# Kernel tuning notes

Hardware: AMD Instinct MI355X
Metric: run time of the kernel (lower is better)

Reference implementation:

```python
import jax, jax.numpy as jnp
import numpy as np


def _lstm_scan(xs, W_ih, W_hh, b, h0, c0):
    """Run an LSTMCell over time. xs: [T, B, D]; returns (hs [T,B,H], h_T, c_T).
    PyTorch LSTMCell gate order: i, f, g, o; b = b_ih + b_hh fused."""
    H = h0.shape[-1]

    def step(carry, x_t):
        h, c = carry
        gates = x_t @ W_ih.T + h @ W_hh.T + b  # [B, 4H]
        i, f, g, o = jnp.split(gates, 4, axis=-1)
        i = jax.nn.sigmoid(i)
        f = jax.nn.sigmoid(f)
        g = jnp.tanh(g)
        o = jax.nn.sigmoid(o)
        c_new = f * c + i * g
        h_new = o * jnp.tanh(c_new)
        return (h_new, c_new), h_new

    (h_T, c_T), hs = jax.lax.scan(step, (h0, c0), xs)
    return hs, h_T, c_T


def setup_inputs() -> dict:
    key = jax.random.key(0)
    ks = jax.random.split(key, 7)
    B, T, F, H = 64, 512, 256, 1024
    s = lambda fan_in: np.sqrt(2.0) * np.sqrt(6.0 / (4 * H + fan_in))  # xavier_uniform gain=sqrt(2)
    return {
        "x": jax.random.normal(ks[0], (B, T, F), dtype=jnp.float32),
        "W_ih_e": jax.random.uniform(ks[1], (4 * H, F), jnp.float32, -s(F), s(F)),
        "W_hh_e": jax.random.uniform(ks[2], (4 * H, H), jnp.float32, -s(H), s(H)),
        "b_e": jnp.zeros((4 * H,), jnp.float32),
        "W_ih_d": jax.random.uniform(ks[3], (4 * H, H), jnp.float32, -s(H), s(H)),
        "W_hh_d": jax.random.uniform(ks[4], (4 * H, H), jnp.float32, -s(H), s(H)),
        "b_d": jnp.zeros((4 * H,), jnp.float32),
        "W_out": jax.random.uniform(ks[5], (F, H), jnp.float32, -s(F), s(F)),
        "b_out": jnp.zeros((F,), jnp.float32),
    }


def reference(x, W_ih_e, W_hh_e, b_e, W_ih_d, W_hh_d, b_d, W_out, b_out):
    B, T, F = x.shape
    H = W_hh_e.shape[1]
    xs = jnp.swapaxes(x, 0, 1)  # [T, B, F] time-major
    h0 = jnp.zeros((B, H), x.dtype)
    c0 = jnp.zeros((B, H), x.dtype)
    # Encoder: LSTMCell(F, H), collect per-step hidden states
    enc_hs, h_T, c_T = _lstm_scan(xs, W_ih_e, W_hh_e, b_e, h0, c0)  # [T, B, H]
    # Decoder: LSTMCell(H, H) over encoder hidden states, seeded with final (h, c)
    dec_hs, _, _ = _lstm_scan(enc_hs, W_ih_d, W_hh_d, b_d, h_T, c_T)  # [T, B, H]
    # Output projection H -> F
    out = jnp.einsum('tbh,fh->tbf', dec_hs, W_out) + b_out
    return jnp.swapaxes(out, 0, 1)  # [B, T, F]
```

## Files before the change

kernel.cpp:

```cpp
#include <hip/hip_runtime.h>
#include <math.h>

#define TT 512
#define BB 64
#define FF 256
#define HH 1024
#define NBLK 256
#define NCHE 5
#define NCHD 8

typedef __attribute__((ext_vector_type(8))) short short8;
typedef __attribute__((ext_vector_type(4))) float f32x4;

__device__ __forceinline__ unsigned short f2bf(float f) {
    unsigned u = __float_as_uint(f);
    u += 0x7FFFu + ((u >> 16) & 1u);
    return (unsigned short)(u >> 16);
}
__device__ __forceinline__ float bf2f(unsigned short u) {
    return __uint_as_float((unsigned)u << 16);
}

__global__ __launch_bounds__(256) void k_cast_x(const float* __restrict__ x,
                                                unsigned short* __restrict__ xB) {
    int t = blockIdx.x;
    #pragma unroll
    for (int i = 0; i < 16; ++i) {
        int id = threadIdx.x + i * 256;
        int b  = id >> 6;
        int f4 = (id & 63) << 2;
        float4 v = *(const float4*)(x + ((size_t)b * TT + t) * FF + f4);
        ushort4 o;
        o.x = f2bf(v.x); o.y = f2bf(v.y); o.z = f2bf(v.z); o.w = f2bf(v.w);
        *(ushort4*)(xB + ((size_t)t * BB + b) * FF + f4) = o;
    }
}

__global__ __launch_bounds__(256) void k_wcast(const float* __restrict__ in,
                                               unsigned short* __restrict__ out,
                                               int n4) {
    int stride = gridDim.x * 256;
    for (int i = blockIdx.x * 256 + threadIdx.x; i < n4; i += stride) {
        float4 v = ((const float4*)in)[i];
        ushort4 o;
        o.x = f2bf(v.x); o.y = f2bf(v.y); o.z = f2bf(v.z); o.w = f2bf(v.w);
        ((ushort4*)out)[i] = o;
    }
}

__device__ __forceinline__ void publish(unsigned* __restrict__ flags,
                                        int widx, unsigned val) {
    asm volatile("s_waitcnt vmcnt(0)" ::: "memory");
    if ((threadIdx.x & 63) == 0)
        __hip_atomic_store(flags + widx, val, __ATOMIC_RELAXED,
                           __HIP_MEMORY_SCOPE_AGENT);
}

__device__ __forceinline__ void waitall16(const unsigned* __restrict__ mir,
                                          int mpage, int lane, unsigned tgt) {
    const unsigned long long* line =
        (const unsigned long long*)(mir + mpage * 64);
    for (;;) {
        unsigned long long v = __hip_atomic_load(line + (lane & 7),
                                                 __ATOMIC_RELAXED,
                                                 __HIP_MEMORY_SCOPE_AGENT);
        bool ok = ((unsigned)v >= tgt) && ((unsigned)(v >> 32) >= tgt);
        if (__all(ok)) break;
        __builtin_amdgcn_s_sleep(1);
    }
    asm volatile("" ::: "memory");
}

__device__ __forceinline__ void aggregator(unsigned* __restrict__ flags,
                                           unsigned* __restrict__ mir,
                                           int g, int lane) {
    for (unsigned e = 1; e <= 2u * TT - 1; ++e) {
        for (;;) {
            unsigned v = __hip_atomic_load(flags + g * 64 + lane,
                                           __ATOMIC_RELAXED,
                                           __HIP_MEMORY_SCOPE_AGENT);
            if (__all(v >= e)) break;
            __builtin_amdgcn_s_sleep(1);
        }
        if (lane < 8)
            __hip_atomic_store(mir + lane * 64 + g, e, __ATOMIC_RELAXED,
                               __HIP_MEMORY_SCOPE_AGENT);
        asm volatile("s_waitcnt vmcnt(0)" ::: "memory");
    }
}

template <int NCH, int C1>
__device__ __forceinline__ void lstm_step(
    const short8* __restrict__ sW,
    const unsigned short* __restrict__ A1, int K1,
    const unsigned short* __restrict__ A2, int K2,
    const f32x4 bias, float& creg,
    unsigned short* __restrict__ hOut,
    unsigned* __restrict__ flags, unsigned* __restrict__ mir,
    int tgt, int widx, unsigned pub, int mpage,
    int lane, int q, int n, int j0, int u, int b)
{
    short8 av[3][8];
    auto aload = [&](short8* dst, int c) {
        const unsigned short* ap = (c < C1)
            ? A1 + (size_t)b * K1 + (size_t)c * 256
            : A2 + (size_t)b * K2 + (size_t)(c - C1) * 256;
        ap += q * 8;
        #pragma unroll
        for (int f = 0; f < 8; ++f) dst[f] = *(const short8*)(ap + f * 32);
    };

    f32x4 accA = {0.f, 0.f, 0.f, 0.f};
    f32x4 accB = {0.f, 0.f, 0.f, 0.f};

    aload(av[0], 0);
    if (C1 > 1) aload(av[1], 1);
    #pragma unroll
    for (int c = 0; c < C1; ++c) {
        if (c + 2 < C1) aload(av[(c + 2) % 3], c + 2);
        const short8* cur = av[c % 3];
        #pragma unroll
        for (int f = 0; f < 8; ++f) {
            short8 wv = sW[(c * 8 + f) * 64 + lane];
            if (f & 1) accB = __builtin_amdgcn_mfma_f32_16x16x32_bf16(wv, cur[f], accB, 0, 0, 0);
            else       accA = __builtin_amdgcn_mfma_f32_16x16x32_bf16(wv, cur[f], accA, 0, 0, 0);
        }
    }

    if (tgt > 0) waitall16(mir, mpage, lane, (unsigned)tgt);

    if (NCH > C1) {
        aload(av[C1 % 3], C1);
        if (NCH > C1 + 1) aload(av[(C1 + 1) % 3], C1 + 1);
        #pragma unroll
        for (int c = C1; c < NCH; ++c) {
            if (c + 2 < NCH) aload(av[(c + 2) % 3], c + 2);
            const short8* cur = av[c % 3];
            #pragma unroll
            for (int f = 0; f < 8; ++f) {
                short8 wv = sW[(c * 8 + f) * 64 + lane];
                if (f & 1) accB = __builtin_amdgcn_mfma_f32_16x16x32_bf16(wv, cur[f], accB, 0, 0, 0);
                else       accA = __builtin_amdgcn_mfma_f32_16x16x32_bf16(wv, cur[f], accA, 0, 0, 0);
            }
        }
    }
    f32x4 acc = accA + accB;

    float pi = acc[0] + bias[0];
    float pf = acc[1] + bias[1];
    float pg = acc[2] + bias[2];
    float po = acc[3] + bias[3];
    float iv = 1.f / (1.f + __expf(-pi));
    float fv = 1.f / (1.f + __expf(-pf));
    float gv = tanhf(pg);
    float ov = 1.f / (1.f + __expf(-po));
    float cn = fv * creg + iv * gv;
    creg = cn;
    float hn = ov * tanhf(cn);

    unsigned hv = (unsigned)f2bf(hn);
    unsigned v0 = (unsigned)__shfl((int)hv, n);
    unsigned v1 = (unsigned)__shfl((int)hv, n + 16);
    unsigned v2 = (unsigned)__shfl((int)hv, n + 32);
    unsigned v3 = (unsigned)__shfl((int)hv, n + 48);
    if (q == 0) {
        unsigned long long pk = (unsigned long long)(v0 | (v1 << 16)) |
                                ((unsigned long long)(v2 | (v3 << 16)) << 32);
        __hip_atomic_store((unsigned long long*)(hOut + (size_t)b * HH + j0), pk,
                           __ATOMIC_RELAXED, __HIP_MEMORY_SCOPE_AGENT);
    }
    if (pub) publish(flags, widx, pub);
}

__global__ __launch_bounds__(320, 1) void k_lstm_persist(
    const unsigned short* __restrict__ xB,
    const unsigned short* __restrict__ WihE,
    const unsigned short* __restrict__ WhhE,
    const float* __restrict__ bE,
    const unsigned short* __restrict__ WihD,
    const unsigned short* __restrict__ WhhD,
    const float* __restrict__ bD,
    unsigned short* __restrict__ encB,
    unsigned short* __restrict__ decR,
    unsigned* __restrict__ flags)
{
    __shared__ short8 sWe[NCHE * 8 * 64];
    __shared__ short8 sWd[NCHD * 8 * 64];

    const int tid  = threadIdx.x;
    const int lane = tid & 63;
    const int w    = tid >> 6;
    unsigned* mir  = flags + 1024;

    if (w == 4) {
        __syncthreads();
        if ((blockIdx.x & 15) == 0)
            aggregator(flags, mir, blockIdx.x >> 4, lane);
        return;
    }

    const int q    = lane >> 4;
    const int n    = lane & 15;
    const int j0   = blockIdx.x * 4;
    const int rrow = (n & 3) * HH + j0 + (n >> 2);
    const size_t SB = (size_t)BB * HH;
    const int widx  = blockIdx.x * 4 + w;
    const int mpage = blockIdx.x & 7;

    #pragma unroll
    for (int i = 0; i < 2 * NCHE; ++i) {
        int g = i * 4 + w;
        int c = g >> 3, f = g & 7;
        const unsigned short* Wp; int Ks; int cl;
        if (c < 1) { Wp = WihE; Ks = FF; cl = c; }
        else       { Wp = WhhE; Ks = HH; cl = c - 1; }
        sWe[g * 64 + lane] =
            *(const short8*)(Wp + (size_t)rrow * Ks + (size_t)cl * 256 + f * 32 + q * 8);
    }
    #pragma unroll
    for (int i = 0; i < 2 * NCHD; ++i) {
        int g = i * 4 + w;
        int c = g >> 3, f = g & 7;
        const unsigned short* Wp; int cl;
        if (c < 4) { Wp = WihD; cl = c; }
        else       { Wp = WhhD; cl = c - 4; }
        sWd[g * 64 + lane] =
            *(const short8*)(Wp + (size_t)rrow * HH + (size_t)cl * 256 + f * 32 + q * 8);
    }
    __syncthreads();

    const int u = j0 + q;
    const int b = w * 16 + n;
    const f32x4 biasE = {bE[u], bE[HH + u], bE[2 * HH + u], bE[3 * HH + u]};
    const f32x4 biasD = {bD[u], bD[HH + u], bD[2 * HH + u], bD[3 * HH + u]};

    float creg = 0.f;

    lstm_step<1, 1>(sWe, xB, FF, xB, FF, biasE, creg,
                    encB, flags, mir, 0, widx, 1u, mpage,
                    lane, q, n, j0, u, b);
    for (int t = 1; t < TT; ++t) {
        lstm_step<NCHE, 1>(sWe, xB + (size_t)t * BB * FF, FF,
                           encB + (size_t)(t - 1) * SB, HH,
                           biasE, creg, encB + (size_t)t * SB,
                           flags, mir, t, widx, (unsigned)(t + 1), mpage,
                           lane, q, n, j0, u, b);
    }

    for (int t = 0; t < TT; ++t) {
        const unsigned short* A2 = (t == 0) ? encB + (size_t)(TT - 1) * SB
                                            : decR + (size_t)(t - 1) * SB;
        unsigned pub = (t == TT - 1) ? 0u : (unsigned)(TT + t + 1);
        lstm_step<NCHD, 4>(sWd, encB + (size_t)t * SB, HH, A2, HH,
                           biasD, creg, decR + (size_t)t * SB,
                           flags, mir, TT + t, widx, pub, mpage,
                           lane, q, n, j0, u, b);
    }
}

__global__ __launch_bounds__(256) void k_out_proj_r(
    const unsigned short* __restrict__ decR,
    const float* __restrict__ Wout,
    const float* __restrict__ bout,
    float* __restrict__ out)
{
    int t  = blockIdx.x;
    int fg = blockIdx.y;
    const int lane = threadIdx.x & 63;
    const int wv   = __builtin_amdgcn_readfirstlane(threadIdx.x >> 6);
    const int f0   = fg * 64 + wv * 16;
    const unsigned short* a = decR + ((size_t)t * BB + lane) * HH;

    float acc[16];
    #pragma unroll
    for (int i = 0; i < 16; ++i) acc[i] = bout[f0 + i];

    for (int k8 = 0; k8 < HH / 8; ++k8) {
        short8 hv8 = *(const short8*)(a + k8 * 8);
        #pragma unroll
        for (int uu = 0; uu < 8; ++uu) {
            float hv = bf2f((unsigned short)hv8[uu]);
            #pragma unroll
            for (int i = 0; i < 16; ++i)
                acc[i] = fmaf(Wout[(size_t)(f0 + i) * HH + k8 * 8 + uu], hv, acc[i]);
        }
    }

    float* op = out + ((size_t)lane * TT + t) * FF + f0;
    #pragma unroll
    for (int i = 0; i < 16; i += 4) {
        float4 v = make_float4(acc[i], acc[i + 1], acc[i + 2], acc[i + 3]);
        *(float4*)(op + i) = v;
    }
}

template <int NCH>
__global__ __launch_bounds__(256) void k_step_lds(
    const unsigned short* __restrict__ A1, const unsigned short* __restrict__ W1, int K1,
    const unsigned short* __restrict__ A2, const unsigned short* __restrict__ W2, int K2,
    int C1,
    const float* __restrict__ bias,
    float* __restrict__ Cbuf,
    unsigned short* __restrict__ hOut,
    float* __restrict__ chunkOut)
{
    __shared__ short8 sW[NCH * 8 * 64];

    const int tid  = threadIdx.x;
    const int lane = tid & 63;
    const int w    = tid >> 6;
    const int q    = lane >> 4;
    const int n    = lane & 15;
    const int j0   = blockIdx.x * 4;
    const int rrow = (n & 3) * HH + j0 + (n >> 2);

    short8 av[3][8];

    auto aload = [&](short8* dst, int c) {
        const unsigned short* ap = (c < C1)
            ? A1 + (size_t)(w * 16 + n) * K1 + (size_t)c * 256
            : A2 + (size_t)(w * 16 + n) * K2 + (size_t)(c - C1) * 256;
        ap += q * 8;
        #pragma unroll
        for (int f = 0; f < 8; ++f) dst[f] = *(const short8*)(ap + f * 32);
    };

    aload(av[0], 0);
    if (NCH > 1) aload(av[1], 1);

    #pragma unroll
    for (int i = 0; i < 2 * NCH; ++i) {
        int g = i * 4 + w;
        int c = g >> 3, f = g & 7;
        const unsigned short* Wp; int Ks; int cl;
        if (c < C1) { Wp = W1; Ks = K1; cl = c; }
        else        { Wp = W2; Ks = K2; cl = c - C1; }
        sW[g * 64 + lane] =
            *(const short8*)(Wp + (size_t)rrow * Ks + (size_t)cl * 256 + f * 32 + q * 8);
    }
    __syncthreads();

    f32x4 accA = {0.f, 0.f, 0.f, 0.f};
    f32x4 accB = {0.f, 0.f, 0.f, 0.f};
    #pragma unroll
    for (int c = 0; c < NCH; ++c) {
        if (c + 2 < NCH) aload(av[(c + 2) % 3], c + 2);
        const short8* cur = av[c % 3];
        #pragma unroll
        for (int f = 0; f < 8; ++f) {
            short8 wv = sW[(c * 8 + f) * 64 + lane];
            if (f & 1) accB = __builtin_amdgcn_mfma_f32_16x16x32_bf16(wv, cur[f], accB, 0, 0, 0);
            else       accA = __builtin_amdgcn_mfma_f32_16x16x32_bf16(wv, cur[f], accA, 0, 0, 0);
        }
    }
    f32x4 acc = accA + accB;

    const int u = j0 + q;
    const int b = w * 16 + n;
    float pi = acc[0] + bias[u];
    float pf = acc[1] + bias[HH + u];
    float pg = acc[2] + bias[2 * HH + u];
    float po = acc[3] + bias[3 * HH + u];
    float iv = 1.f / (1.f + __expf(-pi));
    float fv = 1.f / (1.f + __expf(-pf));
    float gv = tanhf(pg);
    float ov = 1.f / (1.f + __expf(-po));
    size_t cix = (size_t)u * BB + b;
    float c  = Cbuf[cix];
    float cn = fv * c + iv * gv;
    Cbuf[cix] = cn;
    float hn = ov * tanhf(cn);
    hOut[(size_t)b * HH + u] = f2bf(hn);
    if (chunkOut) chunkOut[cix] = hn;
}

__device__ __forceinline__ void seg_f32(const unsigned short* __restrict__ ap0,
                                        const float* __restrict__ wp0,
                                        int nch, f32x4& acc) {
    const unsigned short* ap = ap0;
    const float* wp = wp0;
    #pragma unroll 2
    for (int c = 0; c < nch; ++c) {
        float4 wa = *(const float4*)wp;
        float4 wb = *(const float4*)(wp + 4);
        short8 av = *(const short8*)ap;
        short8 wv;
        wv[0] = (short)f2bf(wa.x); wv[1] = (short)f2bf(wa.y);
        wv[2] = (short)f2bf(wa.z); wv[3] = (short)f2bf(wa.w);
        wv[4] = (short)f2bf(wb.x); wv[5] = (short)f2bf(wb.y);
        wv[6] = (short)f2bf(wb.z); wv[7] = (short)f2bf(wb.w);
        acc = __builtin_amdgcn_mfma_f32_16x16x32_bf16(wv, av, acc, 0, 0, 0);
        ap += 32; wp += 32;
    }
}

__global__ __launch_bounds__(256) void k_step_f32w(
    const unsigned short* __restrict__ A1, const float* __restrict__ W1, int K1,
    const unsigned short* __restrict__ A2, const float* __restrict__ W2, int K2,
    const float* __restrict__ bias,
    float* __restrict__ Cbuf, unsigned short* __restrict__ hOut,
    float* __restrict__ chunkOut)
{
    const int tid  = threadIdx.x;
    const int lane = tid & 63;
    const int w    = tid >> 6;
    const int q    = lane >> 4;
    const int n    = lane & 15;
    const int j0   = blockIdx.x * 4;
    const int rrow = (n & 3) * HH + j0 + (n >> 2);

    f32x4 acc = {0.f, 0.f, 0.f, 0.f};
    seg_f32(A1 + (size_t)(w * 16 + n) * K1 + q * 8,
            W1 + (size_t)rrow * K1 + q * 8, K1 >> 5, acc);
    if (K2)
        seg_f32(A2 + (size_t)(w * 16 + n) * HH + q * 8,
                W2 + (size_t)rrow * HH + q * 8, HH >> 5, acc);

    const int u = j0 + q;
    const int b = w * 16 + n;
    float pi = acc[0] + bias[u];
    float pf = acc[1] + bias[HH + u];
    float pg = acc[2] + bias[2 * HH + u];
    float po = acc[3] + bias[3 * HH + u];
    float iv = 1.f / (1.f + __expf(-pi));
    float fv = 1.f / (1.f + __expf(-pf));
    float gv = tanhf(pg);
    float ov = 1.f / (1.f + __expf(-po));
    size_t cix = (size_t)u * BB + b;
    float c  = Cbuf[cix];
    float cn = fv * c + iv * gv;
    Cbuf[cix] = cn;
    float hn = ov * tanhf(cn);
    hOut[(size_t)b * HH + u] = f2bf(hn);
    if (chunkOut) chunkOut[cix] = hn;
}

__global__ __launch_bounds__(256) void k_out_proj(
    const float* __restrict__ chunk,
    const float* __restrict__ Wout,
    const float* __restrict__ bout,
    float* __restrict__ out,
    int t0)
{
    int tl = blockIdx.x;
    int t  = t0 + tl;
    int fg = blockIdx.y;
    const int lane = threadIdx.x & 63;
    const int wv   = __builtin_amdgcn_readfirstlane(threadIdx.x >> 6);
    const int f0   = fg * 64 + wv * 16;
    const float* a = chunk + (size_t)tl * HH * BB;

    float acc[16];
    #pragma unroll
    for (int i = 0; i < 16; ++i) acc[i] = bout[f0 + i];

    for (int k = 0; k < HH; k += 4) {
        #pragma unroll
        for (int u = 0; u < 4; ++u) {
            float hv = a[(size_t)(k + u) * BB + lane];
            #pragma unroll
            for (int i = 0; i < 16; ++i)
                acc[i] = fmaf(Wout[(size_t)(f0 + i) * HH + k + u], hv, acc[i]);
        }
    }

    float* op = out + ((size_t)lane * TT + t) * FF + f0;
    #pragma unroll
    for (int i = 0; i < 16; i += 4) {
        float4 v = make_float4(acc[i], acc[i + 1], acc[i + 2], acc[i + 3]);
        *(float4*)(op + i) = v;
    }
}

extern "C" void kernel_launch(void* const* d_in, const int* in_sizes, int n_in,
                              void* d_out, int out_size, void* d_ws, size_t ws_size,
                              hipStream_t stream) {
    const float* x     = (const float*)d_in[0];
    const float* Wih_e = (const float*)d_in[1];
    const float* Whh_e = (const float*)d_in[2];
    const float* b_e   = (const float*)d_in[3];
    const float* Wih_d = (const float*)d_in[4];
    const float* Whh_d = (const float*)d_in[5];
    const float* b_d   = (const float*)d_in[6];
    const float* Wout  = (const float*)d_in[7];
    const float* bout  = (const float*)d_in[8];
    float* out = (float*)d_out;

    const size_t SB = (size_t)BB * HH;

    unsigned short* xB = (unsigned short*)d_out;

    {
        char* p = (char*)d_ws;
        unsigned* flags = (unsigned*)p; p += 8192;
        unsigned short* encB  = (unsigned short*)p; p += (size_t)TT * SB * 2;
        unsigned short* decR  = (unsigned short*)p; p += (size_t)TT * SB * 2;
        unsigned short* WihEb = (unsigned short*)p; p += (size_t)4 * HH * FF * 2;
        unsigned short* WhhEb = (unsigned short*)p; p += (size_t)4 * HH * HH * 2;
        unsigned short* WihDb = (unsigned short*)p; p += (size_t)4 * HH * HH * 2;
        unsigned short* WhhDb = (unsigned short*)p; p += (size_t)4 * HH * HH * 2;
        size_t need = (size_t)(p - (char*)d_ws);

        if (ws_size >= need) {
            hipMemsetAsync(flags, 0, 8192, stream);
            k_cast_x<<<TT, 256, 0, stream>>>(x, xB);
            k_wcast<<<1024, 256, 0, stream>>>(Wih_e, WihEb, 4 * HH * FF / 4);
            k_wcast<<<1024, 256, 0, stream>>>(Whh_e, WhhEb, 4 * HH * HH / 4);
            k_wcast<<<1024, 256, 0, stream>>>(Wih_d, WihDb, 4 * HH * HH / 4);
            k_wcast<<<1024, 256, 0, stream>>>(Whh_d, WhhDb, 4 * HH * HH / 4);

            void* args[] = {
                (void*)&xB, (void*)&WihEb, (void*)&WhhEb, (void*)&b_e,
                (void*)&WihDb, (void*)&WhhDb, (void*)&b_d,
                (void*)&encB, (void*)&decR, (void*)&flags};
            hipLaunchCooperativeKernel((const void*)k_lstm_persist,
                                       dim3(NBLK), dim3(320), args, 0, stream);

            k_out_proj_r<<<dim3(TT, 4), 256, 0, stream>>>(decR, Wout, bout, out);
            return;
        }
    }

    char* p = (char*)d_ws;
    unsigned short* encB  = (unsigned short*)p; p += (size_t)TT * SB * 2;
    unsigned short* dech0 = (unsigned short*)p; p += SB * 2;
    unsigned short* dech1 = (unsigned short*)p; p += SB * 2;
    float* cbuf = (float*)p; p += SB * 4;
    size_t used  = (size_t)(p - (char*)d_ws);
    size_t avail = ws_size > used ? ws_size - used : 0;

    const size_t WE_B = ((size_t)4 * HH * FF + (size_t)4 * HH * HH) * 2;
    const size_t WD_B = ((size_t)4 * HH * HH) * 2 * 2;
    const size_t CH8  = (size_t)8 * SB * 4;

    bool wbAll = (avail >= WE_B + WD_B + CH8);
    bool wbEnc = wbAll || (avail >= WE_B + CH8);

    unsigned short *WihEb = 0, *WhhEb = 0, *WihDb = 0, *WhhDb = 0;
    if (wbEnc) {
        WihEb = (unsigned short*)p; p += (size_t)4 * HH * FF * 2;
        WhhEb = (unsigned short*)p; p += (size_t)4 * HH * HH * 2;
        avail -= WE_B;
    }
    if (wbAll) {
        WihDb = (unsigned short*)p; p += (size_t)4 * HH * HH * 2;
        WhhDb = (unsigned short*)p; p += (size_t)4 * HH * HH * 2;
        avail -= WD_B;
    }
    int C = 8;
    if      (avail >= (size_t)64 * SB * 4) C = 64;
    else if (avail >= (size_t)32 * SB * 4) C = 32;
    else if (avail >= (size_t)16 * SB * 4) C = 16;
    float* chunk = (float*)p;

    hipMemsetAsync(cbuf, 0, SB * 4, stream);
    k_cast_x<<<TT, 256, 0, stream>>>(x, xB);
    if (wbEnc) {
        k_wcast<<<1024, 256, 0, stream>>>(Wih_e, WihEb, 4 * HH * FF / 4);
        k_wcast<<<1024, 256, 0, stream>>>(Whh_e, WhhEb, 4 * HH * HH / 4);
    }
    if (wbAll) {
        k_wcast<<<1024, 256, 0, stream>>>(Wih_d, WihDb, 4 * HH * HH / 4);
        k_wcast<<<1024, 256, 0, stream>>>(Whh_d, WhhDb, 4 * HH * HH / 4);
    }

    for (int t = 0; t < TT; ++t) {
        const unsigned short* A1 = xB + (size_t)t * BB * FF;
        const unsigned short* A2 = t ? encB + (size_t)(t - 1) * SB : (unsigned short*)0;
        unsigned short* hOut = encB + (size_t)t * SB;
        if (wbEnc) {
            if (t == 0)
                k_step_lds<1><<<256, 256, 0, stream>>>(A1, WihEb, FF, A2, WhhEb, HH,
                                                       1, b_e, cbuf, hOut, (float*)0);
            else
                k_step_lds<5><<<256, 256, 0, stream>>>(A1, WihEb, FF, A2, WhhEb, HH,
                                                       1, b_e, cbuf, hOut, (float*)0);
        } else {
            k_step_f32w<<<256, 256, 0, stream>>>(A1, Wih_e, FF, A2, Whh_e,
                                                 t ? HH : 0, b_e, cbuf, hOut, (float*)0);
        }
    }

    for (int t = 0; t < TT; ++t) {
        const unsigned short* A1 = encB + (size_t)t * SB;
        const unsigned short* A2 = (t == 0) ? encB + (size_t)(TT - 1) * SB
                                            : ((t & 1) ? dech1 : dech0);
        unsigned short* hOut = ((t + 1) & 1) ? dech1 : dech0;
        int l = t & (C - 1);
        float* ch = chunk + (size_t)l * SB;
        if (wbAll)
            k_step_lds<8><<<256, 256, 0, stream>>>(A1, WihDb, HH, A2, WhhDb, HH,
                                                   4, b_d, cbuf, hOut, ch);
        else
            k_step_f32w<<<256, 256, 0, stream>>>(A1, Wih_d, FF, A2, Whh_d, HH,
                                                 b_d, cbuf, hOut, ch);
        if (l == C - 1)
            k_out_proj<<<dim3(C, 4), 256, 0, stream>>>(chunk, Wout, bout, out,
                                                       t - (C - 1));
    }
}
```

Measured before the change: 10.41 ms.

## Replace aggregator-wave barrier with replicated per-wave flag planes polled directly

Removes the dedicated aggregator wave that collected per-wave flags and republished them to mirror pages. Each wave now writes its step counter into 8 replicated flag planes, and consumers poll one plane (256 flags per wave index) directly before the recurrent part of the GEMM. This drops one hop of flag-propagation latency per timestep and the extra wave. In exchange each waiter polls more cache lines per spin, and each publish does 8 stores instead of one.

```diff
diff --git a/kernel.cpp b/kernel.cpp
--- a/kernel.cpp
+++ b/kernel.cpp
@@ -8,6 +8,7 @@
 #define NBLK 256
 #define NCHE 5
 #define NCHD 8
+#define NMIR 8
 
 typedef __attribute__((ext_vector_type(8))) short short8;
 typedef __attribute__((ext_vector_type(4))) float f32x4;
@@ -48,45 +49,31 @@
     }
 }
 
-__device__ __forceinline__ void publish(unsigned* __restrict__ flags,
-                                        int widx, unsigned val) {
+__device__ __forceinline__ void pubwave(unsigned* __restrict__ flags,
+                                        int w, int blk, unsigned val, int lane) {
     asm volatile("s_waitcnt vmcnt(0)" ::: "memory");
-    if ((threadIdx.x & 63) == 0)
-        __hip_atomic_store(flags + widx, val, __ATOMIC_RELAXED,
-                           __HIP_MEMORY_SCOPE_AGENT);
-}
-
-__device__ __forceinline__ void waitall16(const unsigned* __restrict__ mir,
-                                          int mpage, int lane, unsigned tgt) {
-    const unsigned long long* line =
-        (const unsigned long long*)(mir + mpage * 64);
+    if (lane < NMIR)
+        __hip_atomic_store(flags + lane * 1024 + w * 256 + blk, val,
+                           __ATOMIC_RELAXED, __HIP_MEMORY_SCOPE_AGENT);
+}
+
+__device__ __forceinline__ void waitplane(const unsigned* __restrict__ flags,
+                                          int mpage, int w, int lane,
+                                          unsigned tgt) {
+    const unsigned* fp = flags + mpage * 1024 + w * 256;
     for (;;) {
-        unsigned long long v = __hip_atomic_load(line + (lane & 7),
-                                                 __ATOMIC_RELAXED,
-                                                 __HIP_MEMORY_SCOPE_AGENT);
-        bool ok = ((unsigned)v >= tgt) && ((unsigned)(v >> 32) >= tgt);
+        bool ok = true;
+        #pragma unroll
+        for (int k = 0; k < 4; ++k) {
+            unsigned v = __hip_atomic_load(fp + k * 64 + lane,
+                                           __ATOMIC_RELAXED,
+                                           __HIP_MEMORY_SCOPE_AGENT);
+            ok &= (v >= tgt);
+        }
         if (__all(ok)) break;
         __builtin_amdgcn_s_sleep(1);
     }
     asm volatile("" ::: "memory");
-}
-
-__device__ __forceinline__ void aggregator(unsigned* __restrict__ flags,
-                                           unsigned* __restrict__ mir,
-                                           int g, int lane) {
-    for (unsigned e = 1; e <= 2u * TT - 1; ++e) {
-        for (;;) {
-            unsigned v = __hip_atomic_load(flags + g * 64 + lane,
-                                           __ATOMIC_RELAXED,
-                                           __HIP_MEMORY_SCOPE_AGENT);
-            if (__all(v >= e)) break;
-            __builtin_amdgcn_s_sleep(1);
-        }
-        if (lane < 8)
-            __hip_atomic_store(mir + lane * 64 + g, e, __ATOMIC_RELAXED,
-                               __HIP_MEMORY_SCOPE_AGENT);
-        asm volatile("s_waitcnt vmcnt(0)" ::: "memory");
-    }
 }
 
 template <int NCH, int C1>
@@ -96,8 +83,8 @@
     const unsigned short* __restrict__ A2, int K2,
     const f32x4 bias, float& creg,
     unsigned short* __restrict__ hOut,
-    unsigned* __restrict__ flags, unsigned* __restrict__ mir,
-    int tgt, int widx, unsigned pub, int mpage,
+    unsigned* __restrict__ flags, unsigned sv,
+    int mpage, int blk, int w,
     int lane, int q, int n, int j0, int u, int b)
 {
     short8 av[3][8];
@@ -127,7 +114,10 @@
         }
     }
 
-    if (tgt > 0) waitall16(mir, mpage, lane, (unsigned)tgt);
+    if (sv) {
+        pubwave(flags, w, blk, sv, lane);
+        waitplane(flags, mpage, w, lane, sv);
+    }
 
     if (NCH > C1) {
         aload(av[C1 % 3], C1);
@@ -169,10 +159,9 @@
         __hip_atomic_store((unsigned long long*)(hOut + (size_t)b * HH + j0), pk,
                            __ATOMIC_RELAXED, __HIP_MEMORY_SCOPE_AGENT);
     }
-    if (pub) publish(flags, widx, pub);
-}
-
-__global__ __launch_bounds__(320, 1) void k_lstm_persist(
+}
+
+__global__ __launch_bounds__(256, 1) void k_lstm_persist(
     const unsigned short* __restrict__ xB,
     const unsigned short* __restrict__ WihE,
     const unsigned short* __restrict__ WhhE,
@@ -190,22 +179,13 @@
     const int tid  = threadIdx.x;
     const int lane = tid & 63;
     const int w    = tid >> 6;
-    unsigned* mir  = flags + 1024;
-
-    if (w == 4) {
-        __syncthreads();
-        if ((blockIdx.x & 15) == 0)
-            aggregator(flags, mir, blockIdx.x >> 4, lane);
-        return;
-    }
-
     const int q    = lane >> 4;
     const int n    = lane & 15;
     const int j0   = blockIdx.x * 4;
     const int rrow = (n & 3) * HH + j0 + (n >> 2);
     const size_t SB = (size_t)BB * HH;
-    const int widx  = blockIdx.x * 4 + w;
-    const int mpage = blockIdx.x & 7;
+    const int blk   = blockIdx.x;
+    const int mpage = blockIdx.x & (NMIR - 1);
 
     #pragma unroll
     for (int i = 0; i < 2 * NCHE; ++i) {
@@ -237,23 +217,21 @@
     float creg = 0.f;
 
     lstm_step<1, 1>(sWe, xB, FF, xB, FF, biasE, creg,
-                    encB, flags, mir, 0, widx, 1u, mpage,
-                    lane, q, n, j0, u, b);
+                    encB, flags, 0u, mpage, blk, w, lane, q, n, j0, u, b);
     for (int t = 1; t < TT; ++t) {
         lstm_step<NCHE, 1>(sWe, xB + (size_t)t * BB * FF, FF,
                            encB + (size_t)(t - 1) * SB, HH,
                            biasE, creg, encB + (size_t)t * SB,
-                           flags, mir, t, widx, (unsigned)(t + 1), mpage,
+                           flags, (unsigned)t, mpage, blk, w,
                            lane, q, n, j0, u, b);
     }
 
     for (int t = 0; t < TT; ++t) {
         const unsigned short* A2 = (t == 0) ? encB + (size_t)(TT - 1) * SB
                                             : decR + (size_t)(t - 1) * SB;
-        unsigned pub = (t == TT - 1) ? 0u : (unsigned)(TT + t + 1);
         lstm_step<NCHD, 4>(sWd, encB + (size_t)t * SB, HH, A2, HH,
                            biasD, creg, decR + (size_t)t * SB,
-                           flags, mir, TT + t, widx, pub, mpage,
+                           flags, (unsigned)(TT + t), mpage, blk, w,
                            lane, q, n, j0, u, b);
     }
 }
@@ -492,7 +470,7 @@
 
     {
         char* p = (char*)d_ws;
-        unsigned* flags = (unsigned*)p; p += 8192;
+        unsigned* flags = (unsigned*)p; p += 32768;
         unsigned short* encB  = (unsigned short*)p; p += (size_t)TT * SB * 2;
         unsigned short* decR  = (unsigned short*)p; p += (size_t)TT * SB * 2;
         unsigned short* WihEb = (unsigned short*)p; p += (size_t)4 * HH * FF * 2;
@@ -502,7 +480,7 @@
         size_t need = (size_t)(p - (char*)d_ws);
 
         if (ws_size >= need) {
-            hipMemsetAsync(flags, 0, 8192, stream);
+            hipMemsetAsync(flags, 0, 32768, stream);
             k_cast_x<<<TT, 256, 0, stream>>>(x, xB);
             k_wcast<<<1024, 256, 0, stream>>>(Wih_e, WihEb, 4 * HH * FF / 4);
             k_wcast<<<1024, 256, 0, stream>>>(Whh_e, WhhEb, 4 * HH * HH / 4);
@@ -514,7 +492,7 @@
                 (void*)&WihDb, (void*)&WhhDb, (void*)&b_d,
                 (void*)&encB, (void*)&decR, (void*)&flags};
             hipLaunchCooperativeKernel((const void*)k_lstm_persist,
-                                       dim3(NBLK), dim3(320), args, 0, stream);
+                                       dim3(NBLK), dim3(256), args, 0, stream);
 
             k_out_proj_r<<<dim3(TT, 4), 256, 0, stream>>>(decR, Wout, bout, out);
             return;
```

After: 11.14 ms. 1.07x slower.
